# Kernel optimization log

Hardware: AMD Instinct MI355X
Metric: run time of the kernel (lower is better)

## Reference

```python
import jax, jax.numpy as jnp
import numpy as np

N = 100000   # node_num
D = 256      # enforce_dim
L = 3        # num_layer
E = 200000   # interactions in update batch
B = 50000    # query pairs
W_DECAY = 1e-06
P = 2 * L + 2          # stacked projections per pair
F = P * P              # pair_wise_feature_dim = 64


def setup_inputs() -> dict:
    key = jax.random.key(0)
    ks = jax.random.split(key, 12)
    std = 1.0 / np.sqrt(D)
    inp = {}
    # random projection tables (layer 0 is the random base; layers 1..L are accumulated state)
    inp['rp0'] = jax.random.normal(ks[0], (N, D), jnp.float32) * std
    inp['rp1'] = jax.random.normal(ks[1], (N, D), jnp.float32) * std
    inp['rp2'] = jax.random.normal(ks[2], (N, D), jnp.float32) * std
    inp['rp3'] = jax.random.normal(ks[3], (N, D), jnp.float32) * std
    # sorted interaction timestamps in [0, 1e6]; next_time = times[-1]
    inp['times'] = jnp.sort(jax.random.uniform(ks[4], (E,), jnp.float32) * 1e6)
    inp['now_time'] = jnp.zeros((1,), jnp.float32)
    # MLP: 64 -> 256 -> 64 (stored as [in, out])
    inp['w1'] = jax.random.normal(ks[5], (F, 4 * F), jnp.float32) * (1.0 / np.sqrt(F))
    inp['b1'] = jnp.zeros((4 * F,), jnp.float32)
    inp['w2'] = jax.random.normal(ks[6], (4 * F, F), jnp.float32) * (1.0 / np.sqrt(4 * F))
    inp['b2'] = jnp.zeros((F,), jnp.float32)
    inp['src_ids'] = jax.random.randint(ks[7], (E,), 0, N, jnp.int32)
    inp['dst_ids'] = jax.random.randint(ks[8], (E,), 0, N, jnp.int32)
    inp['q_src'] = jax.random.randint(ks[9], (B,), 0, N, jnp.int32)
    inp['q_dst'] = jax.random.randint(ks[10], (B,), 0, N, jnp.int32)
    return inp


def _update_and_pairwise(rp0, rp1, rp2, rp3, times, now_time, w1, b1, w2, b2,
                         src_ids, dst_ids, q_src, q_dst):
    next_time = times[-1]
    decay = jnp.exp(-W_DECAY * (next_time - now_time[0]))
    # decay accumulated tables: rp[i] *= decay**i for i >= 1
    rps = [rp0, rp1 * decay, rp2 * decay ** 2, rp3 * decay ** 3]
    tw = jnp.exp(-W_DECAY * (next_time - times))[:, None]   # [E,1]
    # update(): for each layer i (all using the pre-update rp[i-1]):
    #   rp[i][src] += rp[i-1][dst] * tw ; rp[i][dst] += rp[i-1][src] * tw
    new = [rps[0]]
    for i in range(1, L + 1):
        upd = rps[i].at[src_ids].add(rps[i - 1][dst_ids] * tw)
        upd = upd.at[dst_ids].add(rps[i - 1][src_ids] * tw)
        new.append(upd)
    # get_pair_wise_feature()
    src_proj = jnp.stack([r[q_src] for r in new], axis=1)   # [B, L+1, D]
    dst_proj = jnp.stack([r[q_dst] for r in new], axis=1)   # [B, L+1, D]
    proj = jnp.concatenate([src_proj, dst_proj], axis=1)    # [B, P, D]
    gram = jnp.einsum('bpd,bqd->bpq', proj, proj).reshape(proj.shape[0], -1)  # [B, F]
    feat = jnp.log1p(jnp.maximum(gram, 0.0))                # not_scale=False path
    h = jax.nn.relu(feat @ w1 + b1)
    return h @ w2 + b2                                      # [B, F]


def reference(rp0, rp1, rp2, rp3, times, now_time, w1, b1, w2, b2,
              src_ids, dst_ids, q_src, q_dst):
    return _update_and_pairwise(rp0, rp1, rp2, rp3, times, now_time,
                                w1, b1, w2, b2, src_ids, dst_ids, q_src, q_dst)
```

## Files before the change

### kernel.cpp

```cpp
#include <hip/hip_runtime.h>
#include <math.h>

#define D 256
#define WDECAY 1e-6f
#define CHUNK 1024


__global__ __launch_bounds__(256) void hist_kernel(
    const int* __restrict__ src, const int* __restrict__ dst, int E,
    int* __restrict__ cnt)
{
    int i = blockIdx.x * blockDim.x + threadIdx.x;
    if (i < 2 * E) {
        int n = (i < E) ? src[i] : dst[i - E];
        atomicAdd(&cnt[n], 1);
    }
}

__global__ __launch_bounds__(256) void scan_partial(
    const int* __restrict__ cnt, int N, int* __restrict__ bsum)
{
    __shared__ int sdata[256];
    int b = blockIdx.x, t = threadIdx.x;
    int base = b * CHUNK + 4 * t;
    int s = 0;
    if (base + 3 < N) {
        int4 v = *(const int4*)(cnt + base);
        s = v.x + v.y + v.z + v.w;
    } else {
        for (int k = 0; k < 4; ++k)
            if (base + k < N) s += cnt[base + k];
    }
    sdata[t] = s;
    __syncthreads();
    for (int off = 128; off > 0; off >>= 1) {
        if (t < off) sdata[t] += sdata[t + off];
        __syncthreads();
    }
    if (t == 0) bsum[b] = sdata[0];
}

__global__ __launch_bounds__(256) void scan_blocksums(
    int* __restrict__ bsum, int NB, int* __restrict__ row_start, int N)
{
    __shared__ int part[256];
    int t = threadIdx.x;
    int per = (NB + 255) / 256;
    int lo = t * per, hi = lo + per;
    if (hi > NB) hi = NB;
    int s = 0;
    for (int i = lo; i < hi; ++i) s += bsum[i];
    part[t] = s;
    __syncthreads();
    for (int off = 1; off < 256; off <<= 1) {
        int v = (t >= off) ? part[t - off] : 0;
        __syncthreads();
        part[t] += v;
        __syncthreads();
    }
    int base = (t == 0) ? 0 : part[t - 1];
    for (int i = lo; i < hi; ++i) {
        int c = bsum[i];
        bsum[i] = base;
        base += c;
    }
    if (t == 255) row_start[N] = part[255];
}

__global__ __launch_bounds__(256) void scan_apply(
    int* __restrict__ cnt, const int* __restrict__ bsum,
    int* __restrict__ row_start, int N)
{
    __shared__ int part[256];
    int b = blockIdx.x, t = threadIdx.x;
    int base = b * CHUNK + 4 * t;
    int4 v = make_int4(0, 0, 0, 0);
    if (base + 3 < N) {
        v = *(const int4*)(cnt + base);
    } else {
        if (base + 0 < N) v.x = cnt[base + 0];
        if (base + 1 < N) v.y = cnt[base + 1];
        if (base + 2 < N) v.z = cnt[base + 2];
    }
    part[t] = v.x + v.y + v.z + v.w;
    __syncthreads();
    for (int off = 1; off < 256; off <<= 1) {
        int pv = (t >= off) ? part[t - off] : 0;
        __syncthreads();
        part[t] += pv;
        __syncthreads();
    }
    int p = bsum[b] + ((t == 0) ? 0 : part[t - 1]);
    int p0 = p, p1 = p0 + v.x, p2 = p1 + v.y, p3 = p2 + v.z;
    if (base + 0 < N) { row_start[base + 0] = p0; cnt[base + 0] = p0; }
    if (base + 1 < N) { row_start[base + 1] = p1; cnt[base + 1] = p1; }
    if (base + 2 < N) { row_start[base + 2] = p2; cnt[base + 2] = p2; }
    if (base + 3 < N) { row_start[base + 3] = p3; cnt[base + 3] = p3; }
}

__global__ __launch_bounds__(256) void fill_kernel(
    const int* __restrict__ src, const int* __restrict__ dst,
    const float* __restrict__ times, int E,
    int* __restrict__ cursor, int* __restrict__ adj_other,
    float* __restrict__ adj_tw)
{
    int i = blockIdx.x * blockDim.x + threadIdx.x;
    if (i >= 2 * E) return;
    int e = (i < E) ? i : i - E;
    int node  = (i < E) ? src[e] : dst[e];
    int other = (i < E) ? dst[e] : src[e];
    float tlast = times[E - 1];
    float w = expf(-WDECAY * (tlast - times[e]));
    int pos = atomicAdd(&cursor[node], 1);
    adj_other[pos] = other;
    adj_tw[pos] = w;
}

__global__ __launch_bounds__(256) void set_flags(
    const int* __restrict__ qs, const int* __restrict__ qd, int B,
    int* __restrict__ flag)
{
    int i = blockIdx.x * blockDim.x + threadIdx.x;
    if (i < B) {
        flag[qs[i]] = 1;
        flag[qd[i]] = 1;
    }
}

__global__ __launch_bounds__(256) void transpose_w1(
    const float* __restrict__ w1, float* __restrict__ w1t)
{
    int t = blockIdx.x * blockDim.x + threadIdx.x;
    if (t < 64 * 256) {
        int i = t & 63;
        int o = t >> 6;
        w1t[t] = w1[i * 256 + o];
    }
}

__global__ __launch_bounds__(64) void apply_updates(
    const float* __restrict__ rp0, const float* __restrict__ rp1,
    const float* __restrict__ rp2, const float* __restrict__ rp3,
    const float* __restrict__ times, const float* __restrict__ now_time, int E,
    const int* __restrict__ row_start, const int* __restrict__ adj_other,
    const float* __restrict__ adj_tw, const int* __restrict__ flag,
    float* __restrict__ new1, float* __restrict__ new2, float* __restrict__ new3)
{
    int n = blockIdx.x;
    if (!flag[n]) return;
    int l = blockIdx.y;
    int lid = threadIdx.x;
    float tlast = times[E - 1];
    float dec = expf(-WDECAY * (tlast - now_time[0]));

    const float* own; const float* gat; float* outp; float os, gs;
    if (l == 0)      { own = rp1; gat = rp0; outp = new1; os = dec;             gs = 1.f;       }
    else if (l == 1) { own = rp2; gat = rp1; outp = new2; os = dec * dec;       gs = dec;       }
    else             { own = rp3; gat = rp2; outp = new3; os = dec * dec * dec; gs = dec * dec; }

    long long base = (long long)n * D + lid * 4;
    float4 acc = *(const float4*)(own + base);
    acc.x *= os; acc.y *= os; acc.z *= os; acc.w *= os;

    int s = row_start[n];
    int e = row_start[n + 1];
    for (int j = s; j < e; ++j) {
        int o = adj_other[j];
        float w = adj_tw[j] * gs;
        float4 v = *(const float4*)(gat + (long long)o * D + lid * 4);
        acc.x += v.x * w; acc.y += v.y * w; acc.z += v.z * w; acc.w += v.w * w;
    }
    *(float4*)(outp + base) = acc;
}


__global__ __launch_bounds__(64) void gather_gram(
    const float* __restrict__ rp0, const float* __restrict__ new1,
    const float* __restrict__ new2, const float* __restrict__ new3,
    const int* __restrict__ q_src, const int* __restrict__ q_dst,
    float* __restrict__ feat, int B)
{
    __shared__ float proj[8][260];
    int b = blockIdx.x;
    int lid = threadIdx.x;
    long long qs = q_src[b];
    long long qd = q_dst[b];

    const float* tabs[4] = {rp0, new1, new2, new3};
    #pragma unroll
    for (int r = 0; r < 4; ++r) {
        const float* tp = tabs[r];
        float4 v = *(const float4*)(tp + qs * D + lid * 4);
        *(float4*)&proj[r][lid * 4] = v;
        float4 w = *(const float4*)(tp + qd * D + lid * 4);
        *(float4*)&proj[r + 4][lid * 4] = w;
    }
    __syncthreads();

    int p = lid >> 3;
    int q = lid & 7;
    float acc = 0.f;
    #pragma unroll 8
    for (int k = 0; k < 64; ++k) {
        float4 a = *(const float4*)&proj[p][4 * k];
        float4 c = *(const float4*)&proj[q][4 * k];
        acc += a.x * c.x + a.y * c.y + a.z * c.z + a.w * c.w;
    }
    feat[(long long)b * 64 + lid] = log1pf(fmaxf(acc, 0.f));
}


__global__ __launch_bounds__(64) void mlp_kernel(
    const float* __restrict__ feat,
    const float* __restrict__ w1t,
    const float* __restrict__ b1,
    const float* __restrict__ w2,
    const float* __restrict__ b2,
    float* __restrict__ out, int B)
{
    __shared__ float fs[64][68];
    int t = threadIdx.x;
    int p0 = blockIdx.x * 64;

    for (int r = 0; r < 64; ++r) {
        int pi = p0 + r;
        fs[r][t] = (pi < B) ? feat[(long long)pi * 64 + t] : 0.f;
    }
    __syncthreads();

    float f[64];
    #pragma unroll
    for (int i = 0; i < 64; i += 4) {
        float4 v = *(const float4*)&fs[t][i];
        f[i] = v.x; f[i + 1] = v.y; f[i + 2] = v.z; f[i + 3] = v.w;
    }

    float oacc[64];
    #pragma unroll
    for (int ou = 0; ou < 64; ++ou) oacc[ou] = 0.f;

    for (int o = 0; o < 256; ++o) {
        const float* w1r = w1t + o * 64;
        float h = b1[o];
        #pragma unroll
        for (int i = 0; i < 64; ++i) h += f[i] * w1r[i];
        h = fmaxf(h, 0.f);
        const float* w2r = w2 + o * 64;
        #pragma unroll
        for (int ou = 0; ou < 64; ++ou) oacc[ou] += h * w2r[ou];
    }

    int pi = p0 + t;
    if (pi < B) {
        float* op = out + (long long)pi * 64;
        #pragma unroll
        for (int ou = 0; ou < 64; ou += 4) {
            float4 v = make_float4(oacc[ou] + b2[ou], oacc[ou + 1] + b2[ou + 1],
                                   oacc[ou + 2] + b2[ou + 2], oacc[ou + 3] + b2[ou + 3]);
            *(float4*)(op + ou) = v;
        }
    }
}


__global__ __launch_bounds__(256) void init_tables(
    const float* __restrict__ rp1, const float* __restrict__ rp2,
    const float* __restrict__ rp3, const float* __restrict__ times,
    const float* __restrict__ now_time, int E,
    float* __restrict__ new1, float* __restrict__ new2, float* __restrict__ new3,
    long long n4)
{
    float tlast = times[E - 1];
    float dec = expf(-WDECAY * (tlast - now_time[0]));
    float d2 = dec * dec;
    float d3 = d2 * dec;
    const float4* r1 = (const float4*)rp1;
    const float4* r2 = (const float4*)rp2;
    const float4* r3 = (const float4*)rp3;
    float4* n1 = (float4*)new1;
    float4* n2 = (float4*)new2;
    float4* n3 = (float4*)new3;
    long long i = (long long)blockIdx.x * blockDim.x + threadIdx.x;
    long long stride = (long long)gridDim.x * blockDim.x;
    for (; i < n4; i += stride) {
        float4 a = r1[i]; a.x *= dec; a.y *= dec; a.z *= dec; a.w *= dec; n1[i] = a;
        float4 b = r2[i]; b.x *= d2; b.y *= d2; b.z *= d2; b.w *= d2; n2[i] = b;
        float4 c = r3[i]; c.x *= d3; c.y *= d3; c.z *= d3; c.w *= d3; n3[i] = c;
    }
}

__global__ __launch_bounds__(256) void scatter_edges(
    const float* __restrict__ rp0, const float* __restrict__ rp1,
    const float* __restrict__ rp2, const float* __restrict__ times,
    const float* __restrict__ now_time,
    const int* __restrict__ src_ids, const int* __restrict__ dst_ids, int E,
    float* __restrict__ new1, float* __restrict__ new2, float* __restrict__ new3)
{
    int e = blockIdx.x;
    int d = threadIdx.x;
    float tlast = times[E - 1];
    float dec = expf(-WDECAY * (tlast - now_time[0]));
    float d2 = dec * dec;
    float tw = expf(-WDECAY * (tlast - times[e]));
    long long s = src_ids[e];
    long long t = dst_ids[e];
    long long so = s * D + d;
    long long to = t * D + d;
    float a0s = rp0[so], a0t = rp0[to];
    atomicAdd(&new1[so], a0t * tw);
    atomicAdd(&new1[to], a0s * tw);
    float a1s = rp1[so] * dec, a1t = rp1[to] * dec;
    atomicAdd(&new2[so], a1t * tw);
    atomicAdd(&new2[to], a1s * tw);
    float a2s = rp2[so] * d2, a2t = rp2[to] * d2;
    atomicAdd(&new3[so], a2t * tw);
    atomicAdd(&new3[to], a2s * tw);
}

__global__ __launch_bounds__(64) void pair_feature_mlp(
    const float* __restrict__ rp0, const float* __restrict__ new1,
    const float* __restrict__ new2, const float* __restrict__ new3,
    const int* __restrict__ q_src, const int* __restrict__ q_dst,
    const float* __restrict__ w1, const float* __restrict__ b1,
    const float* __restrict__ w2, const float* __restrict__ b2,
    float* __restrict__ out, int B)
{
    __shared__ float proj[8][260];
    __shared__ float feat_s[64];
    __shared__ float h_s[256];

    int b = blockIdx.x;
    int lid = threadIdx.x;
    long long qs = q_src[b];
    long long qd = q_dst[b];

    const float* tabs[4] = {rp0, new1, new2, new3};
    #pragma unroll
    for (int r = 0; r < 4; ++r) {
        const float* tp = tabs[r];
        float4 v = *(const float4*)(tp + qs * D + lid * 4);
        *(float4*)&proj[r][lid * 4] = v;
        float4 w = *(const float4*)(tp + qd * D + lid * 4);
        *(float4*)&proj[r + 4][lid * 4] = w;
    }
    __syncthreads();

    int p = lid >> 3;
    int q = lid & 7;
    float acc = 0.f;
    #pragma unroll 8
    for (int k = 0; k < 64; ++k) {
        float4 a = *(const float4*)&proj[p][4 * k];
        float4 c = *(const float4*)&proj[q][4 * k];
        acc += a.x * c.x + a.y * c.y + a.z * c.z + a.w * c.w;
    }
    feat_s[lid] = log1pf(fmaxf(acc, 0.f));
    __syncthreads();

    float4 hv = *(const float4*)(b1 + 4 * lid);
    #pragma unroll 4
    for (int i = 0; i < 64; ++i) {
        float fv = feat_s[i];
        float4 w = *(const float4*)(w1 + i * 256 + 4 * lid);
        hv.x += fv * w.x; hv.y += fv * w.y; hv.z += fv * w.z; hv.w += fv * w.w;
    }
    *(float4*)&h_s[4 * lid] = make_float4(fmaxf(hv.x, 0.f), fmaxf(hv.y, 0.f),
                                          fmaxf(hv.z, 0.f), fmaxf(hv.w, 0.f));
    __syncthreads();

    float o0 = 0.f, o1 = 0.f, o2 = 0.f, o3 = 0.f;
    #pragma unroll 4
    for (int j = 0; j < 256; j += 4) {
        o0 += h_s[j + 0] * w2[(j + 0) * 64 + lid];
        o1 += h_s[j + 1] * w2[(j + 1) * 64 + lid];
        o2 += h_s[j + 2] * w2[(j + 2) * 64 + lid];
        o3 += h_s[j + 3] * w2[(j + 3) * 64 + lid];
    }
    out[(long long)b * 64 + lid] = b2[lid] + (o0 + o1) + (o2 + o3);
}

extern "C" void kernel_launch(void* const* d_in, const int* in_sizes, int n_in,
                              void* d_out, int out_size, void* d_ws, size_t ws_size,
                              hipStream_t stream)
{
    const float* rp0      = (const float*)d_in[0];
    const float* rp1      = (const float*)d_in[1];
    const float* rp2      = (const float*)d_in[2];
    const float* rp3      = (const float*)d_in[3];
    const float* times    = (const float*)d_in[4];
    const float* now_time = (const float*)d_in[5];
    const float* w1       = (const float*)d_in[6];
    const float* b1       = (const float*)d_in[7];
    const float* w2       = (const float*)d_in[8];
    const float* b2       = (const float*)d_in[9];
    const int*   src_ids  = (const int*)d_in[10];
    const int*   dst_ids  = (const int*)d_in[11];
    const int*   q_src    = (const int*)d_in[12];
    const int*   q_dst    = (const int*)d_in[13];
    float* out = (float*)d_out;

    long long ND = in_sizes[0];
    int N = (int)(ND / D);
    int E = in_sizes[4];
    int B = in_sizes[12];
    int NB = (N + CHUNK - 1) / CHUNK;

    float* new1 = (float*)d_ws;
    float* new2 = new1 + ND;
    float* new3 = new2 + ND;

    size_t base_bytes = (size_t)3 * ND * sizeof(float);
    size_t extra_bytes = (size_t)(2 * N + (N + 1) + 2 * E + NB) * sizeof(int)
                       + (size_t)(2 * E) * sizeof(float)
                       + (size_t)B * 64 * sizeof(float)
                       + (size_t)64 * 256 * sizeof(float);

    if (ws_size >= base_bytes + extra_bytes && NB <= 65536) {
        int* cnt       = (int*)(new3 + ND);
        int* flag      = cnt + N;
        int* row_start = flag + N;
        int* adj_other = row_start + N + 1;
        float* adj_tw  = (float*)(adj_other + 2 * E);
        int* bsum      = (int*)(adj_tw + 2 * E);
        float* feat    = (float*)(bsum + NB);
        float* w1t     = feat + (size_t)B * 64;

        hipMemsetAsync(cnt, 0, (size_t)2 * N * sizeof(int), stream);
        int twoE = 2 * E;
        hist_kernel<<<(twoE + 255) / 256, 256, 0, stream>>>(src_ids, dst_ids, E, cnt);
        set_flags<<<(B + 255) / 256, 256, 0, stream>>>(q_src, q_dst, B, flag);
        transpose_w1<<<64, 256, 0, stream>>>(w1, w1t);
        scan_partial<<<NB, 256, 0, stream>>>(cnt, N, bsum);
        scan_blocksums<<<1, 256, 0, stream>>>(bsum, NB, row_start, N);
        scan_apply<<<NB, 256, 0, stream>>>(cnt, bsum, row_start, N);
        fill_kernel<<<(twoE + 255) / 256, 256, 0, stream>>>(src_ids, dst_ids, times, E,
                                                            cnt, adj_other, adj_tw);
        dim3 grid(N, 3);
        apply_updates<<<grid, 64, 0, stream>>>(rp0, rp1, rp2, rp3, times, now_time, E,
                                               row_start, adj_other, adj_tw, flag,
                                               new1, new2, new3);
        gather_gram<<<B, 64, 0, stream>>>(rp0, new1, new2, new3, q_src, q_dst, feat, B);
        mlp_kernel<<<(B + 63) / 64, 64, 0, stream>>>(feat, w1t, b1, w2, b2, out, B);
    } else {
        long long n4 = ND / 4;
        init_tables<<<2048, 256, 0, stream>>>(rp1, rp2, rp3, times, now_time, E,
                                              new1, new2, new3, n4);
        scatter_edges<<<E, 256, 0, stream>>>(rp0, rp1, rp2, times, now_time,
                                             src_ids, dst_ids, E, new1, new2, new3);
        pair_feature_mlp<<<B, 64, 0, stream>>>(rp0, new1, new2, new3, q_src, q_dst,
                                               w1, b1, w2, b2, out, B);
    }
}
```

Before: 780.0 us.

## Stage MLP weights in shared memory and transpose pair features for coalesced loads

The gram kernel now writes features transposed (feature-major) so each MLP thread reads its 64 inputs with coalesced loads. The MLP kernel moves to 256-thread blocks that stage both weight matrices (128 KB) and b1 in LDS, so the per-row weight accesses become broadcast LDS reads instead of global loads. This changes the layout of the feature buffer, the launch shape and the data reuse pattern. In exchange the gram kernel's stores become strided, occupancy is limited to one block per CU by the LDS footprint, and only about 196 blocks are launched.

```diff
diff --git a/kernel.cpp b/kernel.cpp
--- a/kernel.cpp
+++ b/kernel.cpp
@@ -178,7 +178,7 @@
     const float* __restrict__ rp0, const float* __restrict__ new1,
     const float* __restrict__ new2, const float* __restrict__ new3,
     const int* __restrict__ q_src, const int* __restrict__ q_dst,
-    float* __restrict__ feat, int B)
+    float* __restrict__ featT, int B)
 {
     __shared__ float proj[8][260];
     int b = blockIdx.x;
@@ -206,58 +206,84 @@
         float4 c = *(const float4*)&proj[q][4 * k];
         acc += a.x * c.x + a.y * c.y + a.z * c.z + a.w * c.w;
     }
-    feat[(long long)b * 64 + lid] = log1pf(fmaxf(acc, 0.f));
-}
-
-
-__global__ __launch_bounds__(64) void mlp_kernel(
-    const float* __restrict__ feat,
+    featT[(long long)lid * B + b] = log1pf(fmaxf(acc, 0.f));
+}
+
+
+__global__ __launch_bounds__(256, 1) void mlp_kernel(
+    const float* __restrict__ featT,
     const float* __restrict__ w1t,
     const float* __restrict__ b1,
     const float* __restrict__ w2,
     const float* __restrict__ b2,
     float* __restrict__ out, int B)
 {
-    __shared__ float fs[64][68];
+    __shared__ float w1s[256 * 64];
+    __shared__ float w2s[256 * 64];
+    __shared__ float b1s[256];
     int t = threadIdx.x;
-    int p0 = blockIdx.x * 64;
-
-    for (int r = 0; r < 64; ++r) {
-        int pi = p0 + r;
-        fs[r][t] = (pi < B) ? feat[(long long)pi * 64 + t] : 0.f;
-    }
-    __syncthreads();
+
+    {
+        const float4* w1g = (const float4*)w1t;
+        const float4* w2g = (const float4*)w2;
+        float4* w1d = (float4*)w1s;
+        float4* w2d = (float4*)w2s;
+        #pragma unroll
+        for (int k = 0; k < 16; ++k) {
+            int idx = t + 256 * k;
+            w1d[idx] = w1g[idx];
+            w2d[idx] = w2g[idx];
+        }
+        b1s[t] = b1[t];
+    }
+
+    int pi = blockIdx.x * 256 + t;
+    bool valid = (pi < B);
 
     float f[64];
     #pragma unroll
-    for (int i = 0; i < 64; i += 4) {
-        float4 v = *(const float4*)&fs[t][i];
-        f[i] = v.x; f[i + 1] = v.y; f[i + 2] = v.z; f[i + 3] = v.w;
-    }
-
-    float oacc[64];
+    for (int i = 0; i < 64; ++i)
+        f[i] = valid ? featT[(long long)i * B + pi] : 0.f;
+
+    __syncthreads();
+
+    float4 acc[16];
     #pragma unroll
-    for (int ou = 0; ou < 64; ++ou) oacc[ou] = 0.f;
-
+    for (int k = 0; k < 16; ++k) acc[k] = make_float4(0.f, 0.f, 0.f, 0.f);
+
+    #pragma unroll 2
     for (int o = 0; o < 256; ++o) {
-        const float* w1r = w1t + o * 64;
-        float h = b1[o];
+        const float4* w1r = (const float4*)&w1s[o * 64];
+        float4 s = make_float4(0.f, 0.f, 0.f, 0.f);
         #pragma unroll
-        for (int i = 0; i < 64; ++i) h += f[i] * w1r[i];
+        for (int i = 0; i < 16; ++i) {
+            float4 wv = w1r[i];
+            s.x += f[4 * i + 0] * wv.x;
+            s.y += f[4 * i + 1] * wv.y;
+            s.z += f[4 * i + 2] * wv.z;
+            s.w += f[4 * i + 3] * wv.w;
+        }
+        float h = b1s[o] + (s.x + s.y) + (s.z + s.w);
         h = fmaxf(h, 0.f);
-        const float* w2r = w2 + o * 64;
+        const float4* w2r = (const float4*)&w2s[o * 64];
         #pragma unroll
-        for (int ou = 0; ou < 64; ++ou) oacc[ou] += h * w2r[ou];
-    }
-
-    int pi = p0 + t;
-    if (pi < B) {
+        for (int k = 0; k < 16; ++k) {
+            float4 wv = w2r[k];
+            acc[k].x += h * wv.x;
+            acc[k].y += h * wv.y;
+            acc[k].z += h * wv.z;
+            acc[k].w += h * wv.w;
+        }
+    }
+
+    if (valid) {
         float* op = out + (long long)pi * 64;
         #pragma unroll
-        for (int ou = 0; ou < 64; ou += 4) {
-            float4 v = make_float4(oacc[ou] + b2[ou], oacc[ou + 1] + b2[ou + 1],
-                                   oacc[ou + 2] + b2[ou + 2], oacc[ou + 3] + b2[ou + 3]);
-            *(float4*)(op + ou) = v;
+        for (int k = 0; k < 16; ++k) {
+            float4 bv = *(const float4*)(b2 + 4 * k);
+            float4 v = make_float4(acc[k].x + bv.x, acc[k].y + bv.y,
+                                   acc[k].z + bv.z, acc[k].w + bv.w);
+            *(float4*)(op + 4 * k) = v;
         }
     }
 }
@@ -422,8 +448,8 @@
         int* adj_other = row_start + N + 1;
         float* adj_tw  = (float*)(adj_other + 2 * E);
         int* bsum      = (int*)(adj_tw + 2 * E);
-        float* feat    = (float*)(bsum + NB);
-        float* w1t     = feat + (size_t)B * 64;
+        float* featT   = (float*)(bsum + NB);
+        float* w1t     = featT + (size_t)B * 64;
 
         hipMemsetAsync(cnt, 0, (size_t)2 * N * sizeof(int), stream);
         int twoE = 2 * E;
@@ -439,8 +465,8 @@
         apply_updates<<<grid, 64, 0, stream>>>(rp0, rp1, rp2, rp3, times, now_time, E,
                                                row_start, adj_other, adj_tw, flag,
                                                new1, new2, new3);
-        gather_gram<<<B, 64, 0, stream>>>(rp0, new1, new2, new3, q_src, q_dst, feat, B);
-        mlp_kernel<<<(B + 63) / 64, 64, 0, stream>>>(feat, w1t, b1, w2, b2, out, B);
+        gather_gram<<<B, 64, 0, stream>>>(rp0, new1, new2, new3, q_src, q_dst, featT, B);
+        mlp_kernel<<<(B + 255) / 256, 256, 0, stream>>>(featT, w1t, b1, w2, b2, out, B);
     } else {
         long long n4 = ND / 4;
         init_tables<<<2048, 256, 0, stream>>>(rp1, rp2, rp3, times, now_time, E,
```

After: 682.4 us. -12.5%, faster.

## Register-tile MLP as blocked GEMM with transposed features and shared hidden layer

Applied to the files above, without the earlier changes.

The per-pair MLP kernel, in which one thread did the full 64x256x64 chain for a single pair with 64 threads per block, becomes a 256-thread blocked GEMM. Each thread computes an 8x8 tile of the first layer from a shared feature tile, and writes ReLU outputs to a shared hidden buffer. A 4x4 tile of the second layer is then read from that buffer. The gram kernel now writes features transposed so the MLP load is coalesced, and the w1 transpose kernel is dropped. The change aims to raise arithmetic reuse and cut redundant weight loads, at the cost of about 83KB of shared memory per block, the limit of one block per CU set in launch_bounds, and strided scattered stores in gather_gram.

```diff
diff --git a/kernel.cpp b/kernel.cpp
--- a/kernel.cpp
+++ b/kernel.cpp
@@ -4,6 +4,7 @@
 #define D 256
 #define WDECAY 1e-6f
 #define CHUNK 1024
+#define MLP_P 64
 
 
 __global__ __launch_bounds__(256) void hist_kernel(
@@ -127,17 +128,6 @@
     }
 }
 
-__global__ __launch_bounds__(256) void transpose_w1(
-    const float* __restrict__ w1, float* __restrict__ w1t)
-{
-    int t = blockIdx.x * blockDim.x + threadIdx.x;
-    if (t < 64 * 256) {
-        int i = t & 63;
-        int o = t >> 6;
-        w1t[t] = w1[i * 256 + o];
-    }
-}
-
 __global__ __launch_bounds__(64) void apply_updates(
     const float* __restrict__ rp0, const float* __restrict__ rp1,
     const float* __restrict__ rp2, const float* __restrict__ rp3,
@@ -178,7 +168,7 @@
     const float* __restrict__ rp0, const float* __restrict__ new1,
     const float* __restrict__ new2, const float* __restrict__ new3,
     const int* __restrict__ q_src, const int* __restrict__ q_dst,
-    float* __restrict__ feat, int B)
+    float* __restrict__ featT, int B)
 {
     __shared__ float proj[8][260];
     int b = blockIdx.x;
@@ -206,59 +196,103 @@
         float4 c = *(const float4*)&proj[q][4 * k];
         acc += a.x * c.x + a.y * c.y + a.z * c.z + a.w * c.w;
     }
-    feat[(long long)b * 64 + lid] = log1pf(fmaxf(acc, 0.f));
-}
-
-
-__global__ __launch_bounds__(64) void mlp_kernel(
-    const float* __restrict__ feat,
-    const float* __restrict__ w1t,
+    featT[(long long)lid * B + b] = log1pf(fmaxf(acc, 0.f));
+}
+
+__global__ __launch_bounds__(256, 1) void mlp_kernel(
+    const float* __restrict__ featT,
+    const float* __restrict__ w1,
     const float* __restrict__ b1,
     const float* __restrict__ w2,
     const float* __restrict__ b2,
     float* __restrict__ out, int B)
 {
-    __shared__ float fs[64][68];
+    __shared__ float fsT[64][68];
+    __shared__ float hT[256][65];
     int t = threadIdx.x;
-    int p0 = blockIdx.x * 64;
-
-    for (int r = 0; r < 64; ++r) {
-        int pi = p0 + r;
-        fs[r][t] = (pi < B) ? feat[(long long)pi * 64 + t] : 0.f;
-    }
-    __syncthreads();
-
-    float f[64];
-    #pragma unroll
-    for (int i = 0; i < 64; i += 4) {
-        float4 v = *(const float4*)&fs[t][i];
-        f[i] = v.x; f[i + 1] = v.y; f[i + 2] = v.z; f[i + 3] = v.w;
-    }
-
-    float oacc[64];
-    #pragma unroll
-    for (int ou = 0; ou < 64; ++ou) oacc[ou] = 0.f;
-
-    for (int o = 0; o < 256; ++o) {
-        const float* w1r = w1t + o * 64;
-        float h = b1[o];
+    int p0 = blockIdx.x * MLP_P;
+
+    {
+        int p = t & 63;
+        int gp = p0 + p;
+        bool valid = (gp < B);
         #pragma unroll
-        for (int i = 0; i < 64; ++i) h += f[i] * w1r[i];
-        h = fmaxf(h, 0.f);
-        const float* w2r = w2 + o * 64;
+        for (int r = 0; r < 16; ++r) {
+            int k = (t >> 6) + 4 * r;
+            fsT[k][p] = valid ? featT[(long long)k * B + gp] : 0.f;
+        }
+    }
+    __syncthreads();
+
+    {
+        int tp = t >> 5;
+        int to = t & 31;
+        float acc[8][8];
         #pragma unroll
-        for (int ou = 0; ou < 64; ++ou) oacc[ou] += h * w2r[ou];
-    }
-
-    int pi = p0 + t;
-    if (pi < B) {
-        float* op = out + (long long)pi * 64;
+        for (int i = 0; i < 8; ++i)
+            #pragma unroll
+            for (int j = 0; j < 8; ++j) acc[i][j] = 0.f;
+
+        #pragma unroll 4
+        for (int k = 0; k < 64; ++k) {
+            float4 fA = *(const float4*)&fsT[k][tp * 8];
+            float4 fB = *(const float4*)&fsT[k][tp * 8 + 4];
+            const float* wr = w1 + k * 256 + to;
+            float w[8];
+            #pragma unroll
+            for (int j = 0; j < 8; ++j) w[j] = wr[32 * j];
+            float f0 = fA.x, f1 = fA.y, f2 = fA.z, f3 = fA.w;
+            float f4 = fB.x, f5 = fB.y, f6 = fB.z, f7 = fB.w;
+            #pragma unroll
+            for (int j = 0; j < 8; ++j) {
+                acc[0][j] += f0 * w[j]; acc[1][j] += f1 * w[j];
+                acc[2][j] += f2 * w[j]; acc[3][j] += f3 * w[j];
+                acc[4][j] += f4 * w[j]; acc[5][j] += f5 * w[j];
+                acc[6][j] += f6 * w[j]; acc[7][j] += f7 * w[j];
+            }
+        }
         #pragma unroll
-        for (int ou = 0; ou < 64; ou += 4) {
-            float4 v = make_float4(oacc[ou] + b2[ou], oacc[ou + 1] + b2[ou + 1],
-                                   oacc[ou + 2] + b2[ou + 2], oacc[ou + 3] + b2[ou + 3]);
-            *(float4*)(op + ou) = v;
+        for (int j = 0; j < 8; ++j) {
+            int o = to + 32 * j;
+            float bb = b1[o];
+            #pragma unroll
+            for (int i = 0; i < 8; ++i)
+                hT[o][tp * 8 + i] = fmaxf(acc[i][j] + bb, 0.f);
         }
+    }
+    __syncthreads();
+
+    {
+        int tp2 = t >> 4;
+        int tc  = t & 15;
+        float a0x = 0.f, a0y = 0.f, a0z = 0.f, a0w = 0.f;
+        float a1x = 0.f, a1y = 0.f, a1z = 0.f, a1w = 0.f;
+        float a2x = 0.f, a2y = 0.f, a2z = 0.f, a2w = 0.f;
+        float a3x = 0.f, a3y = 0.f, a3z = 0.f, a3w = 0.f;
+
+        #pragma unroll 4
+        for (int k = 0; k < 256; ++k) {
+            float h0 = hT[k][tp2 * 4 + 0];
+            float h1 = hT[k][tp2 * 4 + 1];
+            float h2 = hT[k][tp2 * 4 + 2];
+            float h3 = hT[k][tp2 * 4 + 3];
+            float4 wv = *(const float4*)&w2[k * 64 + tc * 4];
+            a0x += h0 * wv.x; a0y += h0 * wv.y; a0z += h0 * wv.z; a0w += h0 * wv.w;
+            a1x += h1 * wv.x; a1y += h1 * wv.y; a1z += h1 * wv.z; a1w += h1 * wv.w;
+            a2x += h2 * wv.x; a2y += h2 * wv.y; a2z += h2 * wv.z; a2w += h2 * wv.w;
+            a3x += h3 * wv.x; a3y += h3 * wv.y; a3z += h3 * wv.z; a3w += h3 * wv.w;
+        }
+        float4 bv = *(const float4*)&b2[tc * 4];
+        int gp = p0 + tp2 * 4;
+        float* op = out + (long long)gp * 64 + tc * 4;
+        if (gp + 0 < B) *(float4*)(op + 0 * 64) =
+            make_float4(a0x + bv.x, a0y + bv.y, a0z + bv.z, a0w + bv.w);
+        if (gp + 1 < B) *(float4*)(op + 1 * 64) =
+            make_float4(a1x + bv.x, a1y + bv.y, a1z + bv.z, a1w + bv.w);
+        if (gp + 2 < B) *(float4*)(op + 2 * 64) =
+            make_float4(a2x + bv.x, a2y + bv.y, a2z + bv.z, a2w + bv.w);
+        if (gp + 3 < B) *(float4*)(op + 3 * 64) =
+            make_float4(a3x + bv.x, a3y + bv.y, a3z + bv.z, a3w + bv.w);
     }
 }
 
@@ -412,8 +446,7 @@
     size_t base_bytes = (size_t)3 * ND * sizeof(float);
     size_t extra_bytes = (size_t)(2 * N + (N + 1) + 2 * E + NB) * sizeof(int)
                        + (size_t)(2 * E) * sizeof(float)
-                       + (size_t)B * 64 * sizeof(float)
-                       + (size_t)64 * 256 * sizeof(float);
+                       + (size_t)B * 64 * sizeof(float);
 
     if (ws_size >= base_bytes + extra_bytes && NB <= 65536) {
         int* cnt       = (int*)(new3 + ND);
@@ -422,14 +455,12 @@
         int* adj_other = row_start + N + 1;
         float* adj_tw  = (float*)(adj_other + 2 * E);
         int* bsum      = (int*)(adj_tw + 2 * E);
-        float* feat    = (float*)(bsum + NB);
-        float* w1t     = feat + (size_t)B * 64;
+        float* featT   = (float*)(bsum + NB);
 
         hipMemsetAsync(cnt, 0, (size_t)2 * N * sizeof(int), stream);
         int twoE = 2 * E;
         hist_kernel<<<(twoE + 255) / 256, 256, 0, stream>>>(src_ids, dst_ids, E, cnt);
         set_flags<<<(B + 255) / 256, 256, 0, stream>>>(q_src, q_dst, B, flag);
-        transpose_w1<<<64, 256, 0, stream>>>(w1, w1t);
         scan_partial<<<NB, 256, 0, stream>>>(cnt, N, bsum);
         scan_blocksums<<<1, 256, 0, stream>>>(bsum, NB, row_start, N);
         scan_apply<<<NB, 256, 0, stream>>>(cnt, bsum, row_start, N);
@@ -439,8 +470,9 @@
         apply_updates<<<grid, 64, 0, stream>>>(rp0, rp1, rp2, rp3, times, now_time, E,
                                                row_start, adj_other, adj_tw, flag,
                                                new1, new2, new3);
-        gather_gram<<<B, 64, 0, stream>>>(rp0, new1, new2, new3, q_src, q_dst, feat, B);
-        mlp_kernel<<<(B + 63) / 64, 64, 0, stream>>>(feat, w1t, b1, w2, b2, out, B);
+        gather_gram<<<B, 64, 0, stream>>>(rp0, new1, new2, new3, q_src, q_dst, featT, B);
+        mlp_kernel<<<(B + MLP_P - 1) / MLP_P, 256, 0, stream>>>(featT, w1, b1, w2, b2,
+                                                                out, B);
     } else {
         long long n4 = ND / 4;
         init_tables<<<2048, 256, 0, stream>>>(rp1, rp2, rp3, times, now_time, E,
```

Measured after the change: 682.2 us. 12.5% less time.
